# Optimization experiments

Measured on AMD Instinct MI355X. Metric: run time of the kernel, lower is better.

## Reference

```python
import jax, jax.numpy as jnp
import numpy as np

N = 50000      # nodes
E = 800000     # edges (avg degree 16)
D_IN, D_H, D_OUT = 128, 128, 64


def setup_inputs() -> dict:
    key = jax.random.key(0)
    ks = jax.random.split(key, 12)
    s = 0.05  # weight init scale
    return {
        "x": jax.random.normal(ks[0], (N, D_IN), jnp.float32),
        "edge_index": jax.random.randint(ks[1], (2, E), 0, N, dtype=jnp.int64),
        "Wl0": jax.random.normal(ks[2], (D_H, D_IN), jnp.float32) * s,
        "bl0": jax.random.normal(ks[3], (D_H,), jnp.float32) * s,
        "Wr0": jax.random.normal(ks[4], (D_H, D_IN), jnp.float32) * s,
        "Wl1": jax.random.normal(ks[5], (D_H, D_H), jnp.float32) * s,
        "bl1": jax.random.normal(ks[6], (D_H,), jnp.float32) * s,
        "Wr1": jax.random.normal(ks[7], (D_H, D_H), jnp.float32) * s,
        "Wl2": jax.random.normal(ks[8], (D_OUT, D_H), jnp.float32) * s,
        "bl2": jax.random.normal(ks[9], (D_OUT,), jnp.float32) * s,
        "Wr2": jax.random.normal(ks[10], (D_OUT, D_H), jnp.float32) * s,
    }


def _sage_layer(h, src, dst, Wl, bl, Wr):
    # mean aggregation over incoming neighbors: out[i] = mean_{j in N(i)} h[j]
    n = h.shape[0]
    agg = jax.ops.segment_sum(h[src], dst, num_segments=n)          # [N, D]
    deg = jax.ops.segment_sum(jnp.ones((src.shape[0],), h.dtype), dst,
                              num_segments=n)                        # [N]
    mean = agg / jnp.maximum(deg, 1.0)[:, None]  # empty rows -> 0, matches torch_sparse
    # lin_l(agg) + lin_r(self); lin_r has no bias in PyG SAGEConv
    return mean @ Wl.T + bl + h @ Wr.T


def reference(x, edge_index, Wl0, bl0, Wr0, Wl1, bl1, Wr1, Wl2, bl2, Wr2):
    src, dst = edge_index[1], edge_index[0]  # adj row = dst, col = src
    h = jax.nn.relu(_sage_layer(x, src, dst, Wl0, bl0, Wr0))
    h = jax.nn.relu(_sage_layer(h, src, dst, Wl1, bl1, Wr1))
    h = _sage_layer(h, src, dst, Wl2, bl2, Wr2)
    return jax.nn.log_softmax(h, axis=1)
```

## Files before the change

kernel.cpp:

```cpp
#include <hip/hip_runtime.h>
#include <hip/hip_bf16.h>


typedef __attribute__((ext_vector_type(8))) short bf16x8;
typedef __attribute__((ext_vector_type(4))) float f32x4;

#define NPB 128
#define BCAP 2560
#define EPB 8192
#define EPT 32
#define CPAD 16

__device__ __forceinline__ unsigned short f2bf(float f) {
    unsigned int u = __builtin_bit_cast(unsigned int, f);
    u += 0x7fffu + ((u >> 16) & 1u);
    return (unsigned short)(u >> 16);
}
__device__ __forceinline__ float bf2f(unsigned int bits16) {
    return __builtin_bit_cast(float, bits16 << 16);
}
__device__ __forceinline__ bf16x8 pack8(float4 lo, float4 hi) {
    bf16x8 r;
    r[0] = (short)f2bf(lo.x); r[1] = (short)f2bf(lo.y);
    r[2] = (short)f2bf(lo.z); r[3] = (short)f2bf(lo.w);
    r[4] = (short)f2bf(hi.x); r[5] = (short)f2bf(hi.y);
    r[6] = (short)f2bf(hi.z); r[7] = (short)f2bf(hi.w);
    return r;
}


__global__ __launch_bounds__(256) void distribute_kernel(const int* __restrict__ dst,
                                                         const int* __restrict__ srcv,
                                                         int* __restrict__ gcnt,
                                                         unsigned int* __restrict__ staging,
                                                         int E, int NBc) {
    __shared__ unsigned int stage[EPB];
    __shared__ int hist[400];
    __shared__ int lstart[400];
    __shared__ int gbase[400];
    __shared__ int scanbuf[256];
    int t = threadIdx.x;
    int e0 = blockIdx.x * EPB;
    unsigned int w[EPT];

    for (int b = t; b < NBc + 1; b += 256) hist[b] = 0;
    __syncthreads();

#pragma unroll
    for (int i = 0; i < EPT; ++i) {
        int e = e0 + i * 256 + t;
        unsigned int word = 0xFFFFFFFFu;
        if (e < E) word = ((unsigned int)dst[e] << 16) | (unsigned int)srcv[e];
        w[i] = word;
        int b = (int)(word >> 23); if (b > NBc) b = NBc;
        atomicAdd(&hist[b], 1);
    }
    __syncthreads();

    int b0 = 2 * t, b1 = 2 * t + 1;
    int h0 = (b0 <= NBc) ? hist[b0] : 0;
    int h1 = (b1 <= NBc) ? hist[b1] : 0;
    int pair = h0 + h1;
    scanbuf[t] = pair;
    __syncthreads();
    for (int off = 1; off < 256; off <<= 1) {
        int v = (t >= off) ? scanbuf[t - off] : 0;
        __syncthreads();
        scanbuf[t] += v;
        __syncthreads();
    }
    int excl = scanbuf[t] - pair;
    if (b0 <= NBc) lstart[b0] = excl;
    if (b1 <= NBc) lstart[b1] = excl + h0;
    __syncthreads();

    for (int b = t; b < NBc; b += 256) {
        int h = hist[b];
        gbase[b] = h ? atomicAdd(&gcnt[b * CPAD], h) : 0;
    }
    for (int b = t; b < NBc + 1; b += 256) hist[b] = lstart[b];
    __syncthreads();

#pragma unroll
    for (int i = 0; i < EPT; ++i) {
        unsigned int word = w[i];
        int b = (int)(word >> 23); if (b > NBc) b = NBc;
        int p = atomicAdd(&hist[b], 1);
        stage[p] = word;
    }
    __syncthreads();

    int total = lstart[NBc];
    for (int i = t; i < total; i += 256) {
        unsigned int word = stage[i];
        int b = (int)(word >> 23);
        int gpos = gbase[b] + (i - lstart[b]);
        staging[(size_t)b * BCAP + gpos] = word;
    }
}


__global__ __launch_bounds__(256) void build_kernel(const unsigned int* __restrict__ staging,
                                                    const int* __restrict__ gcnt,
                                                    int* __restrict__ row_ptr,
                                                    int* __restrict__ adj, int N, int NBc) {
    __shared__ int hist[NPB];
    __shared__ int scn[NPB];
    __shared__ int wsum[4];
    int b = blockIdx.x;
    int t = threadIdx.x;
    int n0 = b * NPB;
    int nb = N - n0; if (nb > NPB) nb = NPB;
    int ec = gcnt[b * CPAD];
    const unsigned int* st = staging + (size_t)b * BCAP;

    int a = 0;
    for (int j = t; j < b; j += 256) a += gcnt[j * CPAD];
#pragma unroll
    for (int off = 32; off; off >>= 1) a += __shfl_xor(a, off);
    if ((t & 63) == 0) wsum[t >> 6] = a;
    if (t < NPB) hist[t] = 0;
    __syncthreads();
    int bb = wsum[0] + wsum[1] + wsum[2] + wsum[3];

    for (int i = t; i < ec; i += 256)
        atomicAdd(&hist[(st[i] >> 16) & (NPB - 1)], 1);
    __syncthreads();

    int v = (t < NPB) ? hist[t] : 0;
    if (t < NPB) scn[t] = v;
    __syncthreads();
    for (int off = 1; off < NPB; off <<= 1) {
        int u = (t >= off && t < NPB) ? scn[t - off] : 0;
        __syncthreads();
        if (t < NPB) scn[t] += u;
        __syncthreads();
    }
    if (t < NPB) hist[t] = scn[t] - v;
    if (t < nb) row_ptr[n0 + t] = bb + (scn[t] - v);
    if (b == NBc - 1 && t == 0) row_ptr[N] = bb + ec;
    __syncthreads();

    for (int i = t; i < ec; i += 256) {
        unsigned int pk = st[i];
        int p = atomicAdd(&hist[(pk >> 16) & (NPB - 1)], 1);
        adj[bb + p] = (int)(pk & 0xffffu);
    }
}


__global__ void cast_w_kernel(const float* p0, const float* p1, const float* p2,
                              const float* p3, const float* p4, const float* p5,
                              unsigned short* __restrict__ wbf) {
    int w = blockIdx.x * 256 + threadIdx.x;
    if (w < 40960) {
        const float* src;
        int local;
        if      (w < 8192)  { src = p0; local = w; }
        else if (w < 16384) { src = p1; local = w - 8192; }
        else if (w < 24576) { src = p2; local = w - 16384; }
        else if (w < 32768) { src = p3; local = w - 24576; }
        else if (w < 36864) { src = p4; local = w - 32768; }
        else                { src = p5; local = w - 36864; }
        float2 v = ((const float2*)src)[local];
        unsigned int p = (unsigned int)f2bf(v.x) | ((unsigned int)f2bf(v.y) << 16);
        ((unsigned int*)wbf)[w] = p;
    }
}


template<int AF32>
__global__ __launch_bounds__(256) void gemm_mfma_kernel(const void* __restrict__ Hp,
                                                        const unsigned short* __restrict__ Wl,
                                                        const unsigned short* __restrict__ Wr,
                                                        unsigned short* __restrict__ C,
                                                        int N, int ldC) {
    int wave = threadIdx.x >> 6;
    int lane = threadIdx.x & 63;
    int l15 = lane & 15, quad = lane >> 4;
    int y = blockIdx.y, half = gridDim.y >> 1;
    const unsigned short* W = (y < half) ? Wl : Wr;
    int wrow0 = (y < half ? y : y - half) * 64;
    int col0 = y * 64;
    int m0 = blockIdx.x * 128 + wave * 32;

    int r0 = m0 + l15;      if (r0 > N - 1) r0 = N - 1;
    int r1 = m0 + 16 + l15; if (r1 > N - 1) r1 = N - 1;

    f32x4 acc[2][4] = {};
#pragma unroll
    for (int ks = 0; ks < 4; ++ks) {
        int vidx = ks * 4 + quad;
        bf16x8 a0, a1;
        if constexpr (AF32) {
            const float4* A0 = (const float4*)((const float*)Hp + (size_t)r0 * 128);
            const float4* A1 = (const float4*)((const float*)Hp + (size_t)r1 * 128);
            a0 = pack8(A0[vidx * 2], A0[vidx * 2 + 1]);
            a1 = pack8(A1[vidx * 2], A1[vidx * 2 + 1]);
        } else {
            const bf16x8* A0 = (const bf16x8*)((const unsigned short*)Hp + (size_t)r0 * 128);
            const bf16x8* A1 = (const bf16x8*)((const unsigned short*)Hp + (size_t)r1 * 128);
            a0 = A0[vidx];
            a1 = A1[vidx];
        }
#pragma unroll
        for (int j = 0; j < 4; ++j) {
            const bf16x8* B = (const bf16x8*)(W + (size_t)(wrow0 + j * 16 + l15) * 128);
            bf16x8 b = B[vidx];
            acc[0][j] = __builtin_amdgcn_mfma_f32_16x16x32_bf16(a0, b, acc[0][j], 0, 0, 0);
            acc[1][j] = __builtin_amdgcn_mfma_f32_16x16x32_bf16(a1, b, acc[1][j], 0, 0, 0);
        }
    }

#pragma unroll
    for (int i = 0; i < 2; ++i)
#pragma unroll
        for (int j = 0; j < 4; ++j)
#pragma unroll
            for (int r = 0; r < 4; ++r) {
                int row = m0 + i * 16 + quad * 4 + r;
                if (row < N) {
                    int col = col0 + j * 16 + l15;
                    C[(size_t)row * ldC + col] = f2bf(acc[i][j][r]);
                }
            }
}


__global__ __launch_bounds__(256) void agg_relu_kernel(const unsigned short* __restrict__ C,
                                                       const int* __restrict__ row_ptr,
                                                       const int* __restrict__ adj,
                                                       const float* __restrict__ bias,
                                                       unsigned short* __restrict__ hout, int N) {
    int node = (int)((blockIdx.x * blockDim.x + threadIdx.x) >> 6);
    int lane = threadIdx.x & 63;
    if (node >= N) return;
    int g = lane >> 4;
    int c = lane & 15;
    int beg = row_ptr[node], end = row_ptr[node + 1];
    float p[8] = {};

    int e = beg;
    while (e < end) {
        int cnt = end - e; if (cnt > 64) cnt = 64;
        int ll = lane; if (ll > cnt - 1) ll = cnt - 1;
        int myidx = adj[e + ll];
        int c1 = cnt - 1;
        for (int i = 0; i < cnt; i += 16) {
            int t0 = i + g, t1 = i + 4 + g, t2 = i + 8 + g, t3 = i + 12 + g;
            int s0 = __shfl(myidx, t0 > c1 ? c1 : t0);
            int s1 = __shfl(myidx, t1 > c1 ? c1 : t1);
            int s2 = __shfl(myidx, t2 > c1 ? c1 : t2);
            int s3 = __shfl(myidx, t3 > c1 ? c1 : t3);
            float m0 = t0 < cnt ? 1.f : 0.f;
            float m1 = t1 < cnt ? 1.f : 0.f;
            float m2 = t2 < cnt ? 1.f : 0.f;
            float m3 = t3 < cnt ? 1.f : 0.f;
            bf16x8 v0 = ((const bf16x8*)(C + (size_t)s0 * 256))[c];
            bf16x8 v1 = ((const bf16x8*)(C + (size_t)s1 * 256))[c];
            bf16x8 v2 = ((const bf16x8*)(C + (size_t)s2 * 256))[c];
            bf16x8 v3 = ((const bf16x8*)(C + (size_t)s3 * 256))[c];
#pragma unroll
            for (int k = 0; k < 8; ++k) {
                p[k] += m0 * bf2f((unsigned short)v0[k]);
                p[k] += m1 * bf2f((unsigned short)v1[k]);
                p[k] += m2 * bf2f((unsigned short)v2[k]);
                p[k] += m3 * bf2f((unsigned short)v3[k]);
            }
        }
        e += cnt;
    }

#pragma unroll
    for (int k = 0; k < 8; ++k) {
        p[k] += __shfl_xor(p[k], 16);
        p[k] += __shfl_xor(p[k], 32);
    }

    int deg = end - beg;
    float inv = 1.0f / (float)(deg > 1 ? deg : 1);
    bf16x8 sv = ((const bf16x8*)(C + (size_t)node * 256))[16 + c];
    float4 b0 = ((const float4*)bias)[2 * c];
    float4 b1 = ((const float4*)bias)[2 * c + 1];
    float bb[8] = {b0.x, b0.y, b0.z, b0.w, b1.x, b1.y, b1.z, b1.w};
    bf16x8 o;
#pragma unroll
    for (int k = 0; k < 8; ++k) {
        float v = fmaxf(p[k] * inv + bb[k] + bf2f((unsigned short)sv[k]), 0.f);
        o[k] = (short)f2bf(v);
    }
    if (g == 0)
        ((bf16x8*)(hout + (size_t)node * 128))[c] = o;
}


__global__ __launch_bounds__(256) void final_kernel(const unsigned short* __restrict__ C,
                                                    const int* __restrict__ row_ptr,
                                                    const int* __restrict__ adj,
                                                    const float* __restrict__ bias,
                                                    float* __restrict__ out, int N) {
    int node = (int)((blockIdx.x * blockDim.x + threadIdx.x) >> 6);
    int lane = threadIdx.x & 63;
    if (node >= N) return;
    int g = lane >> 3;
    int c = lane & 7;
    int beg = row_ptr[node], end = row_ptr[node + 1];
    float p[8] = {};

    int e = beg;
    while (e < end) {
        int cnt = end - e; if (cnt > 64) cnt = 64;
        int ll = lane; if (ll > cnt - 1) ll = cnt - 1;
        int myidx = adj[e + ll];
        int c1 = cnt - 1;
        for (int i = 0; i < cnt; i += 16) {
            int ta = i + g, tb = i + 8 + g;
            int sa = __shfl(myidx, ta > c1 ? c1 : ta);
            int sb = __shfl(myidx, tb > c1 ? c1 : tb);
            float ma = ta < cnt ? 1.f : 0.f;
            float mb = tb < cnt ? 1.f : 0.f;
            bf16x8 va = ((const bf16x8*)(C + (size_t)sa * 128))[c];
            bf16x8 vb = ((const bf16x8*)(C + (size_t)sb * 128))[c];
#pragma unroll
            for (int k = 0; k < 8; ++k) {
                p[k] += ma * bf2f((unsigned short)va[k]);
                p[k] += mb * bf2f((unsigned short)vb[k]);
            }
        }
        e += cnt;
    }

#pragma unroll
    for (int k = 0; k < 8; ++k) {
        p[k] += __shfl_xor(p[k], 8);
        p[k] += __shfl_xor(p[k], 16);
        p[k] += __shfl_xor(p[k], 32);
    }

    int deg = end - beg;
    float inv = 1.0f / (float)(deg > 1 ? deg : 1);
    bf16x8 sv = ((const bf16x8*)(C + (size_t)node * 128))[8 + c];
    float4 b0 = ((const float4*)bias)[2 * c];
    float4 b1 = ((const float4*)bias)[2 * c + 1];
    float bb[8] = {b0.x, b0.y, b0.z, b0.w, b1.x, b1.y, b1.z, b1.w};
    float u[8];
#pragma unroll
    for (int k = 0; k < 8; ++k)
        u[k] = p[k] * inv + bb[k] + bf2f((unsigned short)sv[k]);

    float m = u[0];
#pragma unroll
    for (int k = 1; k < 8; ++k) m = fmaxf(m, u[k]);
#pragma unroll
    for (int off = 1; off < 8; off <<= 1) m = fmaxf(m, __shfl_xor(m, off));
    float se = 0.f;
#pragma unroll
    for (int k = 0; k < 8; ++k) se += __expf(u[k] - m);
#pragma unroll
    for (int off = 1; off < 8; off <<= 1) se += __shfl_xor(se, off);
    float ls = __logf(se);

    if (g == 0) {
        float4 o0 = {u[0] - m - ls, u[1] - m - ls, u[2] - m - ls, u[3] - m - ls};
        float4 o1 = {u[4] - m - ls, u[5] - m - ls, u[6] - m - ls, u[7] - m - ls};
        ((float4*)(out + (size_t)node * 64))[2 * c] = o0;
        ((float4*)(out + (size_t)node * 64))[2 * c + 1] = o1;
    }
}


extern "C" void kernel_launch(void* const* d_in, const int* in_sizes, int n_in,
                              void* d_out, int out_size, void* d_ws, size_t ws_size,
                              hipStream_t stream) {
    const float* x   = (const float*)d_in[0];
    const int*   ei  = (const int*)d_in[1];
    const float* Wl0 = (const float*)d_in[2];
    const float* bl0 = (const float*)d_in[3];
    const float* Wr0 = (const float*)d_in[4];
    const float* Wl1 = (const float*)d_in[5];
    const float* bl1 = (const float*)d_in[6];
    const float* Wr1 = (const float*)d_in[7];
    const float* Wl2 = (const float*)d_in[8];
    const float* bl2 = (const float*)d_in[9];
    const float* Wr2 = (const float*)d_in[10];
    float* out = (float*)d_out;

    const int N  = in_sizes[0] / 128;
    const int E  = in_sizes[1] / 2;
    const int NB = (N + NPB - 1) / NPB;

    char* ws = (char*)d_ws;
    auto alloc = [&](size_t bytes) {
        char* p = ws;
        ws += (bytes + 255) & ~(size_t)255;
        return p;
    };
    int*   row_ptr    = (int*)alloc((size_t)(N + 1) * 4);
    int*   adj        = (int*)alloc((size_t)E * 4);
    int*   gcnt       = (int*)alloc((size_t)NB * CPAD * 4);
    unsigned int* staging = (unsigned int*)alloc((size_t)NB * BCAP * 4);
    unsigned short* wbf = (unsigned short*)alloc((size_t)81920 * 2);
    unsigned short* C   = (unsigned short*)alloc((size_t)N * 256 * 2);
    unsigned short* hA  = (unsigned short*)alloc((size_t)N * 128 * 2);
    unsigned short* hB  = (unsigned short*)alloc((size_t)N * 128 * 2);

    const int* dstp = ei;
    const int* srcp = ei + E;

    hipMemsetAsync(gcnt, 0, (size_t)NB * CPAD * 4, stream);
    int distBlocks = (E + EPB - 1) / EPB;
    distribute_kernel<<<distBlocks, 256, 0, stream>>>(dstp, srcp, gcnt, staging, E, NB);
    build_kernel<<<NB, 256, 0, stream>>>(staging, gcnt, row_ptr, adj, N, NB);

    cast_w_kernel<<<160, 256, 0, stream>>>(Wl0, Wr0, Wl1, Wr1, Wl2, Wr2, wbf);
    unsigned short* wl0 = wbf;
    unsigned short* wr0 = wbf + 16384;
    unsigned short* wl1 = wbf + 32768;
    unsigned short* wr1 = wbf + 49152;
    unsigned short* wl2 = wbf + 65536;
    unsigned short* wr2 = wbf + 73728;

    dim3 blk(256);
    int gemmRows = (N + 127) / 128;
    int aggBlocks = (N * 64 + 255) / 256;

    gemm_mfma_kernel<1><<<dim3(gemmRows, 4), blk, 0, stream>>>((const void*)x, wl0, wr0, C, N, 256);
    agg_relu_kernel<<<aggBlocks, blk, 0, stream>>>(C, row_ptr, adj, bl0, hA, N);
    gemm_mfma_kernel<0><<<dim3(gemmRows, 4), blk, 0, stream>>>((const void*)hA, wl1, wr1, C, N, 256);
    agg_relu_kernel<<<aggBlocks, blk, 0, stream>>>(C, row_ptr, adj, bl1, hB, N);
    gemm_mfma_kernel<0><<<dim3(gemmRows, 2), blk, 0, stream>>>((const void*)hB, wl2, wr2, C, N, 128);
    final_kernel<<<aggBlocks, blk, 0, stream>>>(C, row_ptr, adj, bl2, out, N);
}
```

Before: 283.0 us.

## Fuse graph build with first GEMM and casts into combined kernel launches

Merges the edge distribution, the x-to-bf16 cast and the weight cast into one launch, and runs the CSR build blocks alongside the layer-0 GEMM blocks in a second launch. This removes launches and lets the independent work overlap. The GEMM epilogue now stages its tile in LDS so each row is written with 16-byte stores instead of scattered 2-byte stores. x is cast to bf16 once into a new buffer, which costs an extra write and read of x.

```diff
diff --git a/kernel.cpp b/kernel.cpp
--- a/kernel.cpp
+++ b/kernel.cpp
@@ -19,28 +19,59 @@
 __device__ __forceinline__ float bf2f(unsigned int bits16) {
     return __builtin_bit_cast(float, bits16 << 16);
 }
-__device__ __forceinline__ bf16x8 pack8(float4 lo, float4 hi) {
-    bf16x8 r;
-    r[0] = (short)f2bf(lo.x); r[1] = (short)f2bf(lo.y);
-    r[2] = (short)f2bf(lo.z); r[3] = (short)f2bf(lo.w);
-    r[4] = (short)f2bf(hi.x); r[5] = (short)f2bf(hi.y);
-    r[6] = (short)f2bf(hi.z); r[7] = (short)f2bf(hi.w);
-    return r;
-}
-
-
-__global__ __launch_bounds__(256) void distribute_kernel(const int* __restrict__ dst,
-                                                         const int* __restrict__ srcv,
-                                                         int* __restrict__ gcnt,
-                                                         unsigned int* __restrict__ staging,
-                                                         int E, int NBc) {
+
+
+__global__ __launch_bounds__(256) void dist_cast_kernel(const int* __restrict__ dst,
+                                                        const int* __restrict__ srcv,
+                                                        int* __restrict__ gcnt,
+                                                        unsigned int* __restrict__ staging,
+                                                        int E, int NBc, int DB, int XB,
+                                                        const float* __restrict__ x,
+                                                        unsigned short* __restrict__ xbf,
+                                                        const float* p0, const float* p1,
+                                                        const float* p2, const float* p3,
+                                                        const float* p4, const float* p5,
+                                                        unsigned short* __restrict__ wbf) {
     __shared__ unsigned int stage[EPB];
     __shared__ int hist[400];
     __shared__ int lstart[400];
     __shared__ int gbase[400];
     __shared__ int scanbuf[256];
+    int bid = blockIdx.x;
     int t = threadIdx.x;
-    int e0 = blockIdx.x * EPB;
+
+    if (bid >= DB && bid < DB + XB) {
+        int base = (bid - DB) * 256 + t;
+        int stride = XB * 256;
+        const float2* x2 = (const float2*)x;
+        unsigned int* xo = (unsigned int*)xbf;
+#pragma unroll
+        for (int k = 0; k < 4; ++k) {
+            int idx = base + k * stride;
+            float2 v = x2[idx];
+            xo[idx] = (unsigned int)f2bf(v.x) | ((unsigned int)f2bf(v.y) << 16);
+        }
+        return;
+    }
+    if (bid >= DB + XB) {
+        int w = (bid - DB - XB) * 256 + t;
+        if (w < 40960) {
+            const float* src;
+            int local;
+            if      (w < 8192)  { src = p0; local = w; }
+            else if (w < 16384) { src = p1; local = w - 8192; }
+            else if (w < 24576) { src = p2; local = w - 16384; }
+            else if (w < 32768) { src = p3; local = w - 24576; }
+            else if (w < 36864) { src = p4; local = w - 32768; }
+            else                { src = p5; local = w - 36864; }
+            float2 v = ((const float2*)src)[local];
+            unsigned int p = (unsigned int)f2bf(v.x) | ((unsigned int)f2bf(v.y) << 16);
+            ((unsigned int*)wbf)[w] = p;
+        }
+        return;
+    }
+
+    int e0 = bid * EPB;
     unsigned int w[EPT];
 
     for (int b = t; b < NBc + 1; b += 256) hist[b] = 0;
@@ -100,15 +131,94 @@
 }
 
 
-__global__ __launch_bounds__(256) void build_kernel(const unsigned int* __restrict__ staging,
-                                                    const int* __restrict__ gcnt,
-                                                    int* __restrict__ row_ptr,
-                                                    int* __restrict__ adj, int N, int NBc) {
+template<int GY>
+__device__ __forceinline__ void gemm_body(int mb, int y,
+                                          const unsigned short* __restrict__ H,
+                                          const unsigned short* __restrict__ Wl,
+                                          const unsigned short* __restrict__ Wr,
+                                          unsigned short* __restrict__ C, int N) {
+    __shared__ unsigned short clds[4 * 32 * 68];
+    const int NCOL = GY * 64;
+    const int half = GY >> 1;
+    int wave = threadIdx.x >> 6;
+    int lane = threadIdx.x & 63;
+    int l15 = lane & 15, quad = lane >> 4;
+    const unsigned short* W = (y < half) ? Wl : Wr;
+    int wrow0 = (y < half ? y : y - half) * 64;
+    int col0 = y * 64;
+    int m0 = mb * 128 + wave * 32;
+
+    int r0 = m0 + l15;      if (r0 > N - 1) r0 = N - 1;
+    int r1 = m0 + 16 + l15; if (r1 > N - 1) r1 = N - 1;
+    const bf16x8* A0 = (const bf16x8*)(H + (size_t)r0 * 128);
+    const bf16x8* A1 = (const bf16x8*)(H + (size_t)r1 * 128);
+
+    f32x4 acc[2][4] = {};
+#pragma unroll
+    for (int ks = 0; ks < 4; ++ks) {
+        int vidx = ks * 4 + quad;
+        bf16x8 a0 = A0[vidx];
+        bf16x8 a1 = A1[vidx];
+#pragma unroll
+        for (int j = 0; j < 4; ++j) {
+            const bf16x8* B = (const bf16x8*)(W + (size_t)(wrow0 + j * 16 + l15) * 128);
+            bf16x8 b = B[vidx];
+            acc[0][j] = __builtin_amdgcn_mfma_f32_16x16x32_bf16(a0, b, acc[0][j], 0, 0, 0);
+            acc[1][j] = __builtin_amdgcn_mfma_f32_16x16x32_bf16(a1, b, acc[1][j], 0, 0, 0);
+        }
+    }
+
+    unsigned short* slice = clds + wave * (32 * 68);
+#pragma unroll
+    for (int i = 0; i < 2; ++i)
+#pragma unroll
+        for (int j = 0; j < 4; ++j)
+#pragma unroll
+            for (int r = 0; r < 4; ++r)
+                slice[(i * 16 + quad * 4 + r) * 68 + j * 16 + l15] = f2bf(acc[i][j][r]);
+    __syncthreads();
+
+    int rlo = lane >> 3, j8 = lane & 7;
+#pragma unroll
+    for (int pass = 0; pass < 4; ++pass) {
+        int row_local = pass * 8 + rlo;
+        const unsigned short* p = slice + row_local * 68 + j8 * 8;
+        unsigned long long lo = *(const unsigned long long*)(p);
+        unsigned long long hi = *(const unsigned long long*)(p + 4);
+        int row = m0 + row_local;
+        if (row < N) {
+            unsigned long long* q = (unsigned long long*)(C + (size_t)row * NCOL + col0 + j8 * 8);
+            q[0] = lo;
+            q[1] = hi;
+        }
+    }
+}
+
+
+__global__ __launch_bounds__(256) void build_gemm_kernel(const unsigned int* __restrict__ staging,
+                                                         const int* __restrict__ gcnt,
+                                                         int* __restrict__ row_ptr,
+                                                         int* __restrict__ adj, int N, int NBc,
+                                                         int gemmRows,
+                                                         const unsigned short* __restrict__ H,
+                                                         const unsigned short* __restrict__ Wl,
+                                                         const unsigned short* __restrict__ Wr,
+                                                         unsigned short* __restrict__ C) {
     __shared__ int hist[NPB];
     __shared__ int scn[NPB];
     __shared__ int wsum[4];
-    int b = blockIdx.x;
+    int bid = blockIdx.x;
     int t = threadIdx.x;
+
+    if (bid >= NBc) {
+        int gid = bid - NBc;
+        int mb = gid % gemmRows;
+        int yy = gid / gemmRows;
+        gemm_body<4>(mb, yy, H, Wl, Wr, C, N);
+        return;
+    }
+
+    int b = bid;
     int n0 = b * NPB;
     int nb = N - n0; if (nb > NPB) nb = NPB;
     int ec = gcnt[b * CPAD];
@@ -149,81 +259,13 @@
 }
 
 
-__global__ void cast_w_kernel(const float* p0, const float* p1, const float* p2,
-                              const float* p3, const float* p4, const float* p5,
-                              unsigned short* __restrict__ wbf) {
-    int w = blockIdx.x * 256 + threadIdx.x;
-    if (w < 40960) {
-        const float* src;
-        int local;
-        if      (w < 8192)  { src = p0; local = w; }
-        else if (w < 16384) { src = p1; local = w - 8192; }
-        else if (w < 24576) { src = p2; local = w - 16384; }
-        else if (w < 32768) { src = p3; local = w - 24576; }
-        else if (w < 36864) { src = p4; local = w - 32768; }
-        else                { src = p5; local = w - 36864; }
-        float2 v = ((const float2*)src)[local];
-        unsigned int p = (unsigned int)f2bf(v.x) | ((unsigned int)f2bf(v.y) << 16);
-        ((unsigned int*)wbf)[w] = p;
-    }
-}
-
-
-template<int AF32>
-__global__ __launch_bounds__(256) void gemm_mfma_kernel(const void* __restrict__ Hp,
+template<int GY>
+__global__ __launch_bounds__(256) void gemm_mfma_kernel(const unsigned short* __restrict__ H,
                                                         const unsigned short* __restrict__ Wl,
                                                         const unsigned short* __restrict__ Wr,
                                                         unsigned short* __restrict__ C,
-                                                        int N, int ldC) {
-    int wave = threadIdx.x >> 6;
-    int lane = threadIdx.x & 63;
-    int l15 = lane & 15, quad = lane >> 4;
-    int y = blockIdx.y, half = gridDim.y >> 1;
-    const unsigned short* W = (y < half) ? Wl : Wr;
-    int wrow0 = (y < half ? y : y - half) * 64;
-    int col0 = y * 64;
-    int m0 = blockIdx.x * 128 + wave * 32;
-
-    int r0 = m0 + l15;      if (r0 > N - 1) r0 = N - 1;
-    int r1 = m0 + 16 + l15; if (r1 > N - 1) r1 = N - 1;
-
-    f32x4 acc[2][4] = {};
-#pragma unroll
-    for (int ks = 0; ks < 4; ++ks) {
-        int vidx = ks * 4 + quad;
-        bf16x8 a0, a1;
-        if constexpr (AF32) {
-            const float4* A0 = (const float4*)((const float*)Hp + (size_t)r0 * 128);
-            const float4* A1 = (const float4*)((const float*)Hp + (size_t)r1 * 128);
-            a0 = pack8(A0[vidx * 2], A0[vidx * 2 + 1]);
-            a1 = pack8(A1[vidx * 2], A1[vidx * 2 + 1]);
-        } else {
-            const bf16x8* A0 = (const bf16x8*)((const unsigned short*)Hp + (size_t)r0 * 128);
-            const bf16x8* A1 = (const bf16x8*)((const unsigned short*)Hp + (size_t)r1 * 128);
-            a0 = A0[vidx];
-            a1 = A1[vidx];
-        }
-#pragma unroll
-        for (int j = 0; j < 4; ++j) {
-            const bf16x8* B = (const bf16x8*)(W + (size_t)(wrow0 + j * 16 + l15) * 128);
-            bf16x8 b = B[vidx];
-            acc[0][j] = __builtin_amdgcn_mfma_f32_16x16x32_bf16(a0, b, acc[0][j], 0, 0, 0);
-            acc[1][j] = __builtin_amdgcn_mfma_f32_16x16x32_bf16(a1, b, acc[1][j], 0, 0, 0);
-        }
-    }
-
-#pragma unroll
-    for (int i = 0; i < 2; ++i)
-#pragma unroll
-        for (int j = 0; j < 4; ++j)
-#pragma unroll
-            for (int r = 0; r < 4; ++r) {
-                int row = m0 + i * 16 + quad * 4 + r;
-                if (row < N) {
-                    int col = col0 + j * 16 + l15;
-                    C[(size_t)row * ldC + col] = f2bf(acc[i][j][r]);
-                }
-            }
+                                                        int N) {
+    gemm_body<GY>(blockIdx.x, blockIdx.y, H, Wl, Wr, C, N);
 }
 
 
@@ -399,6 +441,7 @@
     int*   adj        = (int*)alloc((size_t)E * 4);
     int*   gcnt       = (int*)alloc((size_t)NB * CPAD * 4);
     unsigned int* staging = (unsigned int*)alloc((size_t)NB * BCAP * 4);
+    unsigned short* xbf = (unsigned short*)alloc((size_t)N * 128 * 2);
     unsigned short* wbf = (unsigned short*)alloc((size_t)81920 * 2);
     unsigned short* C   = (unsigned short*)alloc((size_t)N * 256 * 2);
     unsigned short* hA  = (unsigned short*)alloc((size_t)N * 128 * 2);
@@ -407,12 +450,6 @@
     const int* dstp = ei;
     const int* srcp = ei + E;
 
-    hipMemsetAsync(gcnt, 0, (size_t)NB * CPAD * 4, stream);
-    int distBlocks = (E + EPB - 1) / EPB;
-    distribute_kernel<<<distBlocks, 256, 0, stream>>>(dstp, srcp, gcnt, staging, E, NB);
-    build_kernel<<<NB, 256, 0, stream>>>(staging, gcnt, row_ptr, adj, N, NB);
-
-    cast_w_kernel<<<160, 256, 0, stream>>>(Wl0, Wr0, Wl1, Wr1, Wl2, Wr2, wbf);
     unsigned short* wl0 = wbf;
     unsigned short* wr0 = wbf + 16384;
     unsigned short* wl1 = wbf + 32768;
@@ -421,13 +458,20 @@
     unsigned short* wr2 = wbf + 73728;
 
     dim3 blk(256);
+    int DB = (E + EPB - 1) / EPB;
+    int XB = (N * 64) / (256 * 4);
     int gemmRows = (N + 127) / 128;
     int aggBlocks = (N * 64 + 255) / 256;
 
-    gemm_mfma_kernel<1><<<dim3(gemmRows, 4), blk, 0, stream>>>((const void*)x, wl0, wr0, C, N, 256);
+    hipMemsetAsync(gcnt, 0, (size_t)NB * CPAD * 4, stream);
+    dist_cast_kernel<<<DB + XB + 160, blk, 0, stream>>>(dstp, srcp, gcnt, staging, E, NB,
+                                                        DB, XB, x, xbf,
+                                                        Wl0, Wr0, Wl1, Wr1, Wl2, Wr2, wbf);
+    build_gemm_kernel<<<NB + gemmRows * 4, blk, 0, stream>>>(staging, gcnt, row_ptr, adj,
+                                                             N, NB, gemmRows, xbf, wl0, wr0, C);
     agg_relu_kernel<<<aggBlocks, blk, 0, stream>>>(C, row_ptr, adj, bl0, hA, N);
-    gemm_mfma_kernel<0><<<dim3(gemmRows, 4), blk, 0, stream>>>((const void*)hA, wl1, wr1, C, N, 256);
+    gemm_mfma_kernel<4><<<dim3(gemmRows, 4), blk, 0, stream>>>(hA, wl1, wr1, C, N);
     agg_relu_kernel<<<aggBlocks, blk, 0, stream>>>(C, row_ptr, adj, bl1, hB, N);
-    gemm_mfma_kernel<0><<<dim3(gemmRows, 2), blk, 0, stream>>>((const void*)hB, wl2, wr2, C, N, 128);
+    gemm_mfma_kernel<2><<<dim3(gemmRows, 2), blk, 0, stream>>>(hB, wl2, wr2, C, N);
     final_kernel<<<aggBlocks, blk, 0, stream>>>(C, row_ptr, adj, bl2, out, N);
 }
```

Result: faster. 267.9 us (-5.3%).
